# Performance work log

Measured on AMD Instinct MI355X. Metric: run time of the kernel, lower is better.

## Reference

```python
import jax, jax.numpy as jnp
import numpy as np

D_MODEL = 768
NUM_HEADS = 12
D_K = D_MODEL // NUM_HEADS


def setup_inputs() -> dict:
    key = jax.random.key(0)
    ks = jax.random.split(key, 12)
    B, S = 2, 2048
    s = 1.0 / np.sqrt(D_MODEL)
    inp = {
        "query": jax.random.normal(ks[0], (B, S, D_MODEL), jnp.float32),
        "key": jax.random.normal(ks[1], (B, S, D_MODEL), jnp.float32),
        "value": jax.random.normal(ks[2], (B, S, D_MODEL), jnp.float32),
        "mask": jnp.ones((B, 1, 1, S), jnp.int32),
        "Wq": jax.random.normal(ks[3], (D_MODEL, D_MODEL), jnp.float32) * s,
        "bq": jax.random.normal(ks[4], (D_MODEL,), jnp.float32) * s,
        "Wk": jax.random.normal(ks[5], (D_MODEL, D_MODEL), jnp.float32) * s,
        "bk": jax.random.normal(ks[6], (D_MODEL,), jnp.float32) * s,
        "Wv": jax.random.normal(ks[7], (D_MODEL, D_MODEL), jnp.float32) * s,
        "bv": jax.random.normal(ks[8], (D_MODEL,), jnp.float32) * s,
        "Wo": jax.random.normal(ks[9], (D_MODEL, D_MODEL), jnp.float32) * s,
        "bo": jax.random.normal(ks[10], (D_MODEL,), jnp.float32) * s,
    }
    return inp


def reference(query, key, value, mask, Wq, bq, Wk, bk, Wv, bv, Wo, bo):
    B, S, _ = query.shape
    def split_heads(x):  # [B,S,D] -> [B,H,S,d_k]
        return x.reshape(B, -1, NUM_HEADS, D_K).transpose(0, 2, 1, 3)
    q = split_heads(query @ Wq + bq)
    k = split_heads(key @ Wk + bk)
    v = split_heads(value @ Wv + bv)
    scores = jnp.einsum("bhqd,bhkd->bhqk", q, k) / jnp.sqrt(jnp.float32(D_K))
    scores = jnp.where(mask == 0, jnp.float32(-1e9), scores)
    attn = jax.nn.softmax(scores, axis=-1)
    # dropout omitted (eval/deterministic reference)
    out = jnp.einsum("bhqk,bhkd->bhqd", attn, v)
    out = out.transpose(0, 2, 1, 3).reshape(B, S, D_MODEL)
    return out @ Wo + bo
```

## Files before the change

kernel.cpp:

```cpp
#include <hip/hip_runtime.h>

#define DMODEL 768
#define NHEAD  12
#define DK     64
#define NB     2
#define SEQ    2048
#define NTOK   (NB*SEQ)
#define GKIT   (DMODEL/32)

using bf16x8 = __attribute__((ext_vector_type(8))) short;
using f32x4  = __attribute__((ext_vector_type(4))) float;

typedef __attribute__((address_space(1))) const unsigned int gas_u32;
typedef __attribute__((address_space(3))) unsigned int las_u32;

__device__ __forceinline__ void gload_lds16(const void* g, void* l) {
  __builtin_amdgcn_global_load_lds((gas_u32*)g, (las_u32*)l, 16, 0, 0);
}

__device__ __forceinline__ unsigned short f2bf(float f) {
  unsigned int u = __builtin_bit_cast(unsigned int, f);
  u = (u + 0x7FFFu + ((u >> 16) & 1u)) >> 16;
  return (unsigned short)u;
}

__device__ __forceinline__ unsigned cvtpk_bf16(float lo, float hi) {
  unsigned r;
  asm volatile("v_cvt_pk_bf16_f32 %0, %1, %2" : "=v"(r) : "v"(lo), "v"(hi));
  return r;
}

__device__ __forceinline__ unsigned exp2pk_bf16(float a, float b) {
  unsigned r;
  float t;
  asm volatile(
      "v_exp_f32 %0, %2\n\t"
      "v_exp_f32 %1, %3\n\t"
      "s_nop 0\n\t"
      "v_cvt_pk_bf16_f32 %0, %0, %1"
      : "=&v"(r), "=&v"(t)
      : "v"(a), "v"(b));
  return r;
}

__global__ __launch_bounds__(256) void prep_kernel(
    const float* __restrict__ q, const float* __restrict__ k, const float* __restrict__ v,
    unsigned short* __restrict__ oq, unsigned short* __restrict__ ok, unsigned short* __restrict__ ov,
    const float* __restrict__ w0, const float* __restrict__ w1,
    const float* __restrict__ w2, const float* __restrict__ w3,
    unsigned short* __restrict__ t0, unsigned short* __restrict__ t1,
    unsigned short* __restrict__ t2, unsigned short* __restrict__ t3,
    const int* __restrict__ mask, float* __restrict__ maskbias) {
  __shared__ unsigned short tile[64][80];
  int bid = blockIdx.x;
  int t = threadIdx.x;
  if (bid < 4608) {
    int z = bid / 1536, blk = bid % 1536;
    const float* in = z == 0 ? q : (z == 1 ? k : v);
    unsigned short* out = z == 0 ? oq : (z == 1 ? ok : ov);
    size_t i = ((size_t)blk * 256 + t) * 8;
    float4 f0 = *(const float4*)(in + i);
    float4 f1 = *(const float4*)(in + i + 4);
    uint4 w;
    w.x = cvtpk_bf16(f0.x, f0.y); w.y = cvtpk_bf16(f0.z, f0.w);
    w.z = cvtpk_bf16(f1.x, f1.y); w.w = cvtpk_bf16(f1.z, f1.w);
    *(uint4*)(out + i) = w;
  } else if (bid < 5328) {
    int wv = bid - 4608;
    int z = wv / 144, r = wv % 144;
    int c0 = (r % 12) * 64, r0 = (r / 12) * 64;
    const float* in = z == 0 ? w0 : z == 1 ? w1 : z == 2 ? w2 : w3;
    unsigned short* out = z == 0 ? t0 : z == 1 ? t1 : z == 2 ? t2 : t3;
    int row = t >> 2, ch = t & 3;
#pragma unroll
    for (int j4 = 0; j4 < 4; ++j4) {
      float4 f = *(const float4*)(in + (size_t)(r0 + row) * DMODEL + c0 + ch * 16 + j4 * 4);
      tile[row][ch * 16 + j4 * 4 + 0] = f2bf(f.x);
      tile[row][ch * 16 + j4 * 4 + 1] = f2bf(f.y);
      tile[row][ch * 16 + j4 * 4 + 2] = f2bf(f.z);
      tile[row][ch * 16 + j4 * 4 + 3] = f2bf(f.w);
    }
    __syncthreads();
    uint4 wA, wB;
    unsigned short* ta = (unsigned short*)&wA;
    unsigned short* tb = (unsigned short*)&wB;
#pragma unroll
    for (int j = 0; j < 8; ++j) { ta[j] = tile[ch * 16 + j][row]; tb[j] = tile[ch * 16 + 8 + j][row]; }
    unsigned short* ob = out + (size_t)(c0 + row) * DMODEL + r0 + ch * 16;
    *(uint4*)ob = wA;
    *(uint4*)(ob + 8) = wB;
  } else {
    for (int i = t; i < NB * SEQ; i += 256)
      maskbias[i] = mask[i] ? 0.f : -1.4426950408889634e9f;
  }
}

__device__ __forceinline__ void gemm_stage64(const unsigned short* A, const unsigned short* BT,
    unsigned short* As, unsigned short* Bs, int rowbase, int colbase, int kt, int wave, int lane) {
  int r = lane >> 2, c = lane & 3;
#pragma unroll
  for (int iss = 0; iss < 2; ++iss) {
    int row = wave * 32 + iss * 16 + r;
    gload_lds16(A + (size_t)(rowbase + row) * DMODEL + kt * 32 + c * 8,
                As + (wave * 32 + iss * 16) * 32);
  }
  int brow = wave * 16 + r;
  gload_lds16(BT + (size_t)(colbase + brow) * DMODEL + kt * 32 + c * 8, Bs + wave * 16 * 32);
}

__device__ __forceinline__ void gemm_core64(const unsigned short* A, const unsigned short* BT,
    char* gsm, int rowbase, int colbase, f32x4 acc[4][2]) {
  unsigned short* AsAll = (unsigned short*)gsm;
  unsigned short* BsAll = (unsigned short*)(gsm + 16384);
  int t = threadIdx.x, lane = t & 63, wave = t >> 6;
  int wr = wave >> 1, wc = wave & 1, l16 = lane & 15, lk = lane >> 4;
  gemm_stage64(A, BT, AsAll, BsAll, rowbase, colbase, 0, wave, lane);
  __builtin_amdgcn_sched_barrier(0);
  asm volatile("s_waitcnt vmcnt(0)" ::: "memory");
  __builtin_amdgcn_s_barrier();
  for (int kt = 0; kt < GKIT; ++kt) {
    int cur = kt & 1;
    if (kt < GKIT - 1) {
      gemm_stage64(A, BT, AsAll + (cur ^ 1) * 4096, BsAll + (cur ^ 1) * 2048,
                   rowbase, colbase, kt + 1, wave, lane);
      __builtin_amdgcn_sched_barrier(0);
      asm volatile("s_waitcnt vmcnt(3)" ::: "memory");
    } else {
      asm volatile("s_waitcnt vmcnt(0)" ::: "memory");
    }
    __builtin_amdgcn_s_barrier();
    __builtin_amdgcn_sched_barrier(0);
    unsigned short* As = AsAll + cur * 4096;
    unsigned short* Bs = BsAll + cur * 2048;
    bf16x8 a[4], bb[2];
#pragma unroll
    for (int m = 0; m < 4; ++m) a[m] = *(const bf16x8*)(As + (wr * 64 + m * 16 + l16) * 32 + lk * 8);
#pragma unroll
    for (int n = 0; n < 2; ++n) bb[n] = *(const bf16x8*)(Bs + (wc * 32 + n * 16 + l16) * 32 + lk * 8);
    __builtin_amdgcn_s_setprio(1);
#pragma unroll
    for (int m = 0; m < 4; ++m)
#pragma unroll
      for (int n = 0; n < 2; ++n)
        acc[m][n] = __builtin_amdgcn_mfma_f32_16x16x32_bf16(a[m], bb[n], acc[m][n], 0, 0, 0);
    __builtin_amdgcn_s_setprio(0);
    __builtin_amdgcn_sched_barrier(0);
    __builtin_amdgcn_s_barrier();
  }
}

struct QKVArgs {
  const unsigned short* A[3];
  const unsigned short* BT[3];
  const float* bias[3];
  unsigned short* out[3];
  float scale;
};

__global__ __launch_bounds__(256) void gemm_qkv_kernel(QKVArgs ga) {
  __shared__ char gsm[24576];
  int bid = blockIdx.x;
  int xcd = bid & 7, idx = bid >> 3;
  int rt = xcd * 4 + idx / 36;
  int ct = idx % 36;
  int z = ct / 12;
  int colbase = (ct % 12) * 64;
  int rowbase = rt * 128;
  f32x4 acc[4][2];
#pragma unroll
  for (int m = 0; m < 4; ++m)
#pragma unroll
    for (int n = 0; n < 2; ++n) acc[m][n] = (f32x4){0.f, 0.f, 0.f, 0.f};
  gemm_core64(ga.A[z], ga.BT[z], gsm, rowbase, colbase, acc);
  const float* bias = ga.bias[z];
  int t = threadIdx.x, lane = t & 63, wave = t >> 6;
  int wr = wave >> 1, wc = wave & 1, l16 = lane & 15, lk = lane >> 4;
  if (z == 2) {
    int hh = colbase >> 6;
#pragma unroll
    for (int n = 0; n < 2; ++n) {
      int c = wc * 32 + n * 16 + l16;
      float bv = bias[colbase + c];
      int swz = (c & 7) << 4;
#pragma unroll
      for (int m = 0; m < 4; ++m) {
        uint2 w;
        w.x = cvtpk_bf16(acc[m][n][0] + bv, acc[m][n][1] + bv);
        w.y = cvtpk_bf16(acc[m][n][2] + bv, acc[m][n][3] + bv);
        int rp = wr * 64 + m * 16 + lk * 4;
        *(uint2*)(gsm + c * 256 + ((rp * 2) ^ swz)) = w;
      }
    }
    __syncthreads();
    int c = t >> 2, ch = t & 3;
    int swz2 = (c & 7) << 4;
    int bb2 = rowbase >> 11;
    unsigned short* dst = ga.out[2] + ((size_t)(bb2 * NHEAD + hh) * DK + c) * SEQ +
                          (rowbase & 2047) + ch * 32;
#pragma unroll
    for (int j = 0; j < 4; ++j) {
      uint4 w = *(const uint4*)(gsm + c * 256 + ((ch * 64 + j * 16) ^ swz2));
      *(uint4*)(dst + j * 8) = w;
    }
  } else {
    float scale = (z == 0) ? ga.scale : 1.f;
    unsigned short* out = ga.out[z];
#pragma unroll
    for (int n = 0; n < 2; ++n) {
      int gcol = colbase + wc * 32 + n * 16 + l16;
      float bv = bias[gcol];
      int h = gcol >> 6, d = gcol & 63;
#pragma unroll
      for (int m = 0; m < 4; ++m) {
        int growb = rowbase + wr * 64 + m * 16 + lk * 4;
#pragma unroll
        for (int i = 0; i < 4; ++i) {
          int grow = growb + i;
          int b = grow >> 11, s = grow & 2047;
          out[((size_t)(b * NHEAD + h) * SEQ + s) * DK + d] = f2bf((acc[m][n][i] + bv) * scale);
        }
      }
    }
  }
}

__global__ __launch_bounds__(256) void gemm_o_kernel(
    const unsigned short* __restrict__ A, const unsigned short* __restrict__ BT,
    const float* __restrict__ bias, float* __restrict__ out) {
  __shared__ char gsm[24576];
  int bid = blockIdx.x;
  int xcd = bid & 7, idx = bid >> 3;
  int rt = xcd * 4 + idx / 12;
  int colbase = (idx % 12) * 64;
  int rowbase = rt * 128;
  f32x4 acc[4][2];
#pragma unroll
  for (int m = 0; m < 4; ++m)
#pragma unroll
    for (int n = 0; n < 2; ++n) acc[m][n] = (f32x4){0.f, 0.f, 0.f, 0.f};
  gemm_core64(A, BT, gsm, rowbase, colbase, acc);
  int lane = threadIdx.x & 63, wave = threadIdx.x >> 6;
  int wr = wave >> 1, wc = wave & 1, l16 = lane & 15, lk = lane >> 4;
#pragma unroll
  for (int n = 0; n < 2; ++n) {
    int gcol = colbase + wc * 32 + n * 16 + l16;
    float bv = bias[gcol];
#pragma unroll
    for (int m = 0; m < 4; ++m) {
      int growb = rowbase + wr * 64 + m * 16 + lk * 4;
#pragma unroll
      for (int i = 0; i < 4; ++i)
        out[(size_t)(growb + i) * DMODEL + gcol] = acc[m][n][i] + bv;
    }
  }
}

template<int SPLIT>
__global__ __launch_bounds__(256, 3) void flash_kernel(
    const unsigned short* __restrict__ Qh, const unsigned short* __restrict__ Kh,
    const unsigned short* __restrict__ Vt, const float* __restrict__ maskbias,
    unsigned short* __restrict__ AO, float* __restrict__ Opart, float* __restrict__ Lpart) {
  constexpr int NT = (SEQ / SPLIT) / 64;
  constexpr int MBI = (SPLIT == 2) ? 1 : 2;
  __shared__ char smem[49152 + MBI * 4096];
  char* Ks = smem;
  char* Vs = smem + 16384;
  char* Ps = smem + 32768;
  float* mbs = (float*)(smem + 49152);

  int orig = blockIdx.x;
  int xcd = orig & 7, idx = orig >> 3;
  int bh, qt, sp;
  if (SPLIT == 2) {
    bh = xcd * 3 + idx / 32;
    int r = idx & 31; qt = r >> 1; sp = r & 1;
  } else {
    bh = xcd * 3 + idx / 16;
    qt = idx & 15; sp = 0;
  }
  int b = bh / NHEAD, h = bh % NHEAD;
  int kv0 = sp * (SEQ / SPLIT);

  int t = threadIdx.x, lane = t & 63, wave = t >> 6;
  int l16 = lane & 15, lk = lane >> 4;
  size_t headQ = (size_t)bh * SEQ * DK;
  size_t headV = (size_t)bh * DK * SEQ;
  int qbase = qt * 128 + wave * 32;

  const unsigned short* Kg = Kh + headQ + (size_t)kv0 * DK;
  const unsigned short* Vg = Vt + headV + kv0;
  const float* mbg = maskbias + b * SEQ + kv0;
  char* Pw = Ps + wave * 4096;

  bf16x8 aq[2][2];
#pragma unroll
  for (int h2 = 0; h2 < 2; ++h2) {
    const unsigned short* qp = Qh + headQ + (size_t)(qbase + h2 * 16 + l16) * DK + lk * 8;
    aq[h2][0] = *(const bf16x8*)qp;
    aq[h2][1] = *(const bf16x8*)(qp + 32);
  }
  bf16x8 ones;
#pragma unroll
  for (int j = 0; j < 8; ++j) ones[j] = (short)0x3F80;

  int sr8 = lane >> 3, sch = lane & 7;
  const unsigned short* KgT = Kg + (size_t)(wave * 16 + sr8) * DK + ((sch ^ sr8) << 3);
  const unsigned short* VgT = Vg + (size_t)(wave * 16 + sr8) * SEQ + ((sch ^ sr8) << 3);
  char* kD0 = Ks + wave * 2048;
  char* vD0 = Vs + wave * 2048;

#pragma unroll
  for (int j = 0; j < MBI; ++j)
    gload_lds16(mbg + (wave * MBI + j) * 256 + lane * 4, (char*)mbs + (wave * MBI + j) * 1024);
  gload_lds16(KgT, kD0);
  gload_lds16(KgT + 512, kD0 + 1024);
  gload_lds16(VgT, vD0);
  gload_lds16(VgT + 8 * SEQ, vD0 + 1024);
  __builtin_amdgcn_sched_barrier(0);
  asm volatile("s_waitcnt vmcnt(0)" ::: "memory");
  __builtin_amdgcn_s_barrier();

  f32x4 o[2][4], lacc[2];
#pragma unroll
  for (int h2 = 0; h2 < 2; ++h2) {
    lacc[h2] = (f32x4){0.f, 0.f, 0.f, 0.f};
#pragma unroll
    for (int t4 = 0; t4 < 4; ++t4) o[h2][t4] = (f32x4){0.f, 0.f, 0.f, 0.f};
  }

  for (int kt = 0; kt < NT; ++kt) {
    int cur = kt & 1;
    if (kt + 1 < NT) {
      const unsigned short* kS = KgT + (size_t)(kt + 1) * 4096;
      const unsigned short* vS = VgT + (kt + 1) * 64;
      char* kD = kD0 + (cur ^ 1) * 8192;
      char* vD = vD0 + (cur ^ 1) * 8192;
      gload_lds16(kS, kD);
      gload_lds16(kS + 512, kD + 1024);
      gload_lds16(vS, vD);
      gload_lds16(vS + 8 * SEQ, vD + 1024);
      __builtin_amdgcn_sched_barrier(0);
      asm volatile("s_waitcnt vmcnt(4)" ::: "memory");
    } else {
      asm volatile("s_waitcnt vmcnt(0)" ::: "memory");
    }
    __builtin_amdgcn_s_barrier();
    __builtin_amdgcn_sched_barrier(0);

    const char* kb = Ks + cur * 8192;
    const char* vb = Vs + cur * 8192;

    f32x4 sv[2][4];
    __builtin_amdgcn_s_setprio(1);
#pragma unroll
    for (int n = 0; n < 4; ++n) {
      f32x4 bias = *(const f32x4*)((const char*)mbs + kt * 256 + n * 64 + lk * 16);
      int key = n * 16 + l16;
      bf16x8 k0 = *(const bf16x8*)(kb + ((key * 128 + lk * 16) ^ ((key & 7) << 4)));
      bf16x8 k1 = *(const bf16x8*)(kb + ((key * 128 + 64 + lk * 16) ^ ((key & 7) << 4)));
#pragma unroll
      for (int h2 = 0; h2 < 2; ++h2) {
        f32x4 zz = __builtin_amdgcn_mfma_f32_16x16x32_bf16(k1, aq[h2][1], bias, 0, 0, 0);
        sv[h2][n] = __builtin_amdgcn_mfma_f32_16x16x32_bf16(k0, aq[h2][0], zz, 0, 0, 0);
      }
    }
    __builtin_amdgcn_s_setprio(0);

#pragma unroll
    for (int h2 = 0; h2 < 2; ++h2)
#pragma unroll
      for (int n = 0; n < 4; ++n) {
        uint2 w;
        w.x = exp2pk_bf16(sv[h2][n][0], sv[h2][n][1]);
        w.y = exp2pk_bf16(sv[h2][n][2], sv[h2][n][3]);
        int qr = h2 * 16 + l16;
        int byt = (qr * 128 + n * 32 + lk * 8) ^ ((qr & 7) << 4);
        *(uint2*)(Pw + byt) = w;
      }

    bf16x8 ap[2][2];
#pragma unroll
    for (int h2 = 0; h2 < 2; ++h2) {
      int qr = h2 * 16 + l16;
      ap[h2][0] = *(const bf16x8*)(Pw + ((qr * 128 + lk * 16) ^ ((qr & 7) << 4)));
      ap[h2][1] = *(const bf16x8*)(Pw + ((qr * 128 + 64 + lk * 16) ^ ((qr & 7) << 4)));
    }

    __builtin_amdgcn_s_setprio(1);
#pragma unroll
    for (int t4 = 0; t4 < 4; ++t4) {
      int d = t4 * 16 + l16;
      bf16x8 bv0 = *(const bf16x8*)(vb + ((d * 128 + lk * 16) ^ ((d & 7) << 4)));
      bf16x8 bv1 = *(const bf16x8*)(vb + ((d * 128 + 64 + lk * 16) ^ ((d & 7) << 4)));
#pragma unroll
      for (int h2 = 0; h2 < 2; ++h2) {
        o[h2][t4] = __builtin_amdgcn_mfma_f32_16x16x32_bf16(ap[h2][0], bv0, o[h2][t4], 0, 0, 0);
        o[h2][t4] = __builtin_amdgcn_mfma_f32_16x16x32_bf16(ap[h2][1], bv1, o[h2][t4], 0, 0, 0);
      }
    }
#pragma unroll
    for (int h2 = 0; h2 < 2; ++h2) {
      lacc[h2] = __builtin_amdgcn_mfma_f32_16x16x32_bf16(ap[h2][0], ones, lacc[h2], 0, 0, 0);
      lacc[h2] = __builtin_amdgcn_mfma_f32_16x16x32_bf16(ap[h2][1], ones, lacc[h2], 0, 0, 0);
    }
    __builtin_amdgcn_s_setprio(0);
    __builtin_amdgcn_sched_barrier(0);
    __builtin_amdgcn_s_barrier();
  }

  if (SPLIT == 2) {
    size_t pb = ((size_t)(bh * 16 + qt) * 2 + sp) * 8192;
#pragma unroll
    for (int h2 = 0; h2 < 2; ++h2)
#pragma unroll
      for (int t4 = 0; t4 < 4; ++t4)
#pragma unroll
        for (int i = 0; i < 4; ++i)
          Opart[pb + (size_t)(wave * 32 + h2 * 16 + lk * 4 + i) * 64 + t4 * 16 + l16] = o[h2][t4][i];
    if (l16 == 0) {
      int qi0 = ((bh * 16 + qt) * 2 + sp) * 128 + wave * 32;
#pragma unroll
      for (int h2 = 0; h2 < 2; ++h2)
#pragma unroll
        for (int i = 0; i < 4; ++i)
          Lpart[qi0 + h2 * 16 + lk * 4 + i] = lacc[h2][i];
    }
  } else {
#pragma unroll
    for (int h2 = 0; h2 < 2; ++h2) {
      f32x4 li;
#pragma unroll
      for (int i = 0; i < 4; ++i) li[i] = 1.0f / lacc[h2][i];
#pragma unroll
      for (int t4 = 0; t4 < 4; ++t4) {
        int col = h * DK + t4 * 16 + l16;
#pragma unroll
        for (int i = 0; i < 4; ++i) {
          int srq = qbase + h2 * 16 + lk * 4 + i;
          AO[(size_t)(b * SEQ + srq) * DMODEL + col] = f2bf(o[h2][t4][i] * li[i]);
        }
      }
    }
  }
}

__global__ __launch_bounds__(256) void merge_kernel(
    const float* __restrict__ Opart, const float* __restrict__ Lpart,
    unsigned short* __restrict__ AO) {
  int blk = blockIdx.x;
  int qh = blk & 1;
  int qt = (blk >> 1) & 15;
  int bh = blk >> 5;
  int b = bh / NHEAD, h = bh % NHEAD;
  int t = threadIdx.x;
  int q = t >> 2, dc = (t & 3) * 16;
  size_t base0 = ((size_t)(bh * 16 + qt) * 2) * 8192 + (size_t)(qh * 64 + q) * 64 + dc;
  const float* o0 = Opart + base0;
  const float* o1 = o0 + 8192;
  int qi = (bh * 16 + qt) * 2 * 128 + qh * 64 + q;
  float l0 = Lpart[qi], l1 = Lpart[qi + 128];
  float linv = 1.f / (l0 + l1);
  int row = qt * 128 + qh * 64 + q;
  unsigned short* dst = AO + ((size_t)(b * SEQ + row)) * DMODEL + h * DK + dc;
#pragma unroll
  for (int j = 0; j < 4; ++j) {
    float4 a = *(const float4*)(o0 + j * 4);
    float4 c = *(const float4*)(o1 + j * 4);
    uint2 w;
    w.x = cvtpk_bf16((a.x + c.x) * linv, (a.y + c.y) * linv);
    w.y = cvtpk_bf16((a.z + c.z) * linv, (a.w + c.w) * linv);
    *(uint2*)(dst + j * 4) = w;
  }
}

extern "C" void kernel_launch(void* const* d_in, const int* in_sizes, int n_in,
                              void* d_out, int out_size, void* d_ws, size_t ws_size,
                              hipStream_t stream) {
  const float* gq  = (const float*)d_in[0];
  const float* gk  = (const float*)d_in[1];
  const float* gv  = (const float*)d_in[2];
  const int* gmask = (const int*)d_in[3];
  const float* gWq = (const float*)d_in[4];
  const float* gbq = (const float*)d_in[5];
  const float* gWk = (const float*)d_in[6];
  const float* gbk = (const float*)d_in[7];
  const float* gWv = (const float*)d_in[8];
  const float* gbv = (const float*)d_in[9];
  const float* gWo = (const float*)d_in[10];
  const float* gbo = (const float*)d_in[11];
  float* out = (float*)d_out;

  char* ws = (char*)d_ws;
  const size_t XSZ = (size_t)NTOK * DMODEL * 2;
  const size_t WSZ = (size_t)DMODEL * DMODEL * 2;
  const size_t OPSZ = (size_t)768 * 8192 * 4;

  float* Opart = (float*)ws;
  unsigned short* Xq = (unsigned short*)ws;
  unsigned short* Xk = Xq + XSZ / 2;
  unsigned short* Xv = Xk + XSZ / 2;
  char* p = ws + OPSZ;
  float* Lpart = (float*)p; p += (size_t)768 * 128 * 4;
  unsigned short* WqT = (unsigned short*)p; p += WSZ;
  unsigned short* WkT = (unsigned short*)p; p += WSZ;
  unsigned short* WvT = (unsigned short*)p; p += WSZ;
  unsigned short* WoT = (unsigned short*)p; p += WSZ;
  unsigned short* Qh  = (unsigned short*)p; p += XSZ;
  unsigned short* Kh  = (unsigned short*)p; p += XSZ;
  unsigned short* Vt  = (unsigned short*)p; p += XSZ;
  unsigned short* AO  = (unsigned short*)p; p += XSZ;
  float* maskbias     = (float*)p; p += (size_t)NB * SEQ * 4;
  size_t needed = (size_t)(p - ws);
  bool split2 = ws_size >= needed;

  prep_kernel<<<dim3(5329), 256, 0, stream>>>(gq, gk, gv, Xq, Xk, Xv,
                                              gWq, gWk, gWv, gWo, WqT, WkT, WvT, WoT,
                                              gmask, maskbias);

  QKVArgs ga;
  ga.A[0] = Xq; ga.A[1] = Xk; ga.A[2] = Xv;
  ga.BT[0] = WqT; ga.BT[1] = WkT; ga.BT[2] = WvT;
  ga.bias[0] = gbq; ga.bias[1] = gbk; ga.bias[2] = gbv;
  ga.out[0] = Qh; ga.out[1] = Kh; ga.out[2] = Vt;
  ga.scale = 0.18033688011112042f;
  gemm_qkv_kernel<<<dim3(1152), 256, 0, stream>>>(ga);

  if (split2) {
    flash_kernel<2><<<dim3(768), 256, 0, stream>>>(Qh, Kh, Vt, maskbias, AO, Opart, Lpart);
    merge_kernel<<<dim3(768), 256, 0, stream>>>(Opart, Lpart, AO);
  } else {
    flash_kernel<1><<<dim3(384), 256, 0, stream>>>(Qh, Kh, Vt, maskbias, AO, Opart, Lpart);
  }
  gemm_o_kernel<<<dim3(384), 256, 0, stream>>>(AO, WoT, gbo, out);
}
```

Baseline: 108.6 us.

## Double GEMM K-tile to 64 with XOR-swizzled LDS layout

The QKV and output projection GEMMs now stage 64-wide K slices per iteration instead of 32. This halves the number of main-loop iterations and barriers. The LDS tile uses an XOR swizzle on 16-byte chunks to avoid bank conflicts on the MFMA operand reads. Shared memory doubles to 48KB, and an occupancy hint of 3 blocks is added, which may limit residency. An extra sync was added before the V epilogue reuses the shared buffer.

```diff
diff --git a/kernel.cpp b/kernel.cpp
--- a/kernel.cpp
+++ b/kernel.cpp
@@ -6,7 +6,7 @@
 #define NB     2
 #define SEQ    2048
 #define NTOK   (NB*SEQ)
-#define GKIT   (DMODEL/32)
+#define GK64   (DMODEL/64)
 
 using bf16x8 = __attribute__((ext_vector_type(8))) short;
 using f32x4  = __attribute__((ext_vector_type(4))) float;
@@ -97,52 +97,68 @@
 
 __device__ __forceinline__ void gemm_stage64(const unsigned short* A, const unsigned short* BT,
     unsigned short* As, unsigned short* Bs, int rowbase, int colbase, int kt, int wave, int lane) {
-  int r = lane >> 2, c = lane & 3;
-#pragma unroll
-  for (int iss = 0; iss < 2; ++iss) {
-    int row = wave * 32 + iss * 16 + r;
-    gload_lds16(A + (size_t)(rowbase + row) * DMODEL + kt * 32 + c * 8,
-                As + (wave * 32 + iss * 16) * 32);
-  }
-  int brow = wave * 16 + r;
-  gload_lds16(BT + (size_t)(colbase + brow) * DMODEL + kt * 32 + c * 8, Bs + wave * 16 * 32);
+  int r8 = lane >> 3, c = lane & 7;
+  int swz = (c ^ r8) << 3;
+#pragma unroll
+  for (int g = 0; g < 4; ++g) {
+    int row = wave * 32 + g * 8 + r8;
+    gload_lds16(A + (size_t)(rowbase + row) * DMODEL + kt * 64 + swz,
+                As + (wave * 32 + g * 8) * 64);
+  }
+#pragma unroll
+  for (int g = 0; g < 2; ++g) {
+    int row = wave * 16 + g * 8 + r8;
+    gload_lds16(BT + (size_t)(colbase + row) * DMODEL + kt * 64 + swz,
+                Bs + (wave * 16 + g * 8) * 64);
+  }
 }
 
 __device__ __forceinline__ void gemm_core64(const unsigned short* A, const unsigned short* BT,
     char* gsm, int rowbase, int colbase, f32x4 acc[4][2]) {
   unsigned short* AsAll = (unsigned short*)gsm;
-  unsigned short* BsAll = (unsigned short*)(gsm + 16384);
+  unsigned short* BsAll = (unsigned short*)(gsm + 32768);
   int t = threadIdx.x, lane = t & 63, wave = t >> 6;
   int wr = wave >> 1, wc = wave & 1, l16 = lane & 15, lk = lane >> 4;
   gemm_stage64(A, BT, AsAll, BsAll, rowbase, colbase, 0, wave, lane);
   __builtin_amdgcn_sched_barrier(0);
   asm volatile("s_waitcnt vmcnt(0)" ::: "memory");
   __builtin_amdgcn_s_barrier();
-  for (int kt = 0; kt < GKIT; ++kt) {
+  for (int kt = 0; kt < GK64; ++kt) {
     int cur = kt & 1;
-    if (kt < GKIT - 1) {
-      gemm_stage64(A, BT, AsAll + (cur ^ 1) * 4096, BsAll + (cur ^ 1) * 2048,
+    if (kt < GK64 - 1) {
+      gemm_stage64(A, BT, AsAll + (cur ^ 1) * 8192, BsAll + (cur ^ 1) * 4096,
                    rowbase, colbase, kt + 1, wave, lane);
       __builtin_amdgcn_sched_barrier(0);
-      asm volatile("s_waitcnt vmcnt(3)" ::: "memory");
+      asm volatile("s_waitcnt vmcnt(6)" ::: "memory");
     } else {
       asm volatile("s_waitcnt vmcnt(0)" ::: "memory");
     }
     __builtin_amdgcn_s_barrier();
     __builtin_amdgcn_sched_barrier(0);
-    unsigned short* As = AsAll + cur * 4096;
-    unsigned short* Bs = BsAll + cur * 2048;
-    bf16x8 a[4], bb[2];
-#pragma unroll
-    for (int m = 0; m < 4; ++m) a[m] = *(const bf16x8*)(As + (wr * 64 + m * 16 + l16) * 32 + lk * 8);
-#pragma unroll
-    for (int n = 0; n < 2; ++n) bb[n] = *(const bf16x8*)(Bs + (wc * 32 + n * 16 + l16) * 32 + lk * 8);
+    const char* As = (const char*)(AsAll + cur * 8192);
+    const char* Bs = (const char*)(BsAll + cur * 4096);
+    bf16x8 a[2][4], bb[2][2];
+#pragma unroll
+    for (int k2 = 0; k2 < 2; ++k2) {
+#pragma unroll
+      for (int m = 0; m < 4; ++m) {
+        int row = wr * 64 + m * 16 + l16;
+        a[k2][m] = *(const bf16x8*)(As + row * 128 + (((k2 * 4 + lk) ^ (row & 7)) << 4));
+      }
+#pragma unroll
+      for (int n = 0; n < 2; ++n) {
+        int row = wc * 32 + n * 16 + l16;
+        bb[k2][n] = *(const bf16x8*)(Bs + row * 128 + (((k2 * 4 + lk) ^ (row & 7)) << 4));
+      }
+    }
     __builtin_amdgcn_s_setprio(1);
 #pragma unroll
-    for (int m = 0; m < 4; ++m)
-#pragma unroll
-      for (int n = 0; n < 2; ++n)
-        acc[m][n] = __builtin_amdgcn_mfma_f32_16x16x32_bf16(a[m], bb[n], acc[m][n], 0, 0, 0);
+    for (int k2 = 0; k2 < 2; ++k2)
+#pragma unroll
+      for (int m = 0; m < 4; ++m)
+#pragma unroll
+        for (int n = 0; n < 2; ++n)
+          acc[m][n] = __builtin_amdgcn_mfma_f32_16x16x32_bf16(a[k2][m], bb[k2][n], acc[m][n], 0, 0, 0);
     __builtin_amdgcn_s_setprio(0);
     __builtin_amdgcn_sched_barrier(0);
     __builtin_amdgcn_s_barrier();
@@ -157,8 +173,8 @@
   float scale;
 };
 
-__global__ __launch_bounds__(256) void gemm_qkv_kernel(QKVArgs ga) {
-  __shared__ char gsm[24576];
+__global__ __launch_bounds__(256, 3) void gemm_qkv_kernel(QKVArgs ga) {
+  __shared__ char gsm[49152];
   int bid = blockIdx.x;
   int xcd = bid & 7, idx = bid >> 3;
   int rt = xcd * 4 + idx / 36;
@@ -176,6 +192,7 @@
   int t = threadIdx.x, lane = t & 63, wave = t >> 6;
   int wr = wave >> 1, wc = wave & 1, l16 = lane & 15, lk = lane >> 4;
   if (z == 2) {
+    __syncthreads();
     int hh = colbase >> 6;
 #pragma unroll
     for (int n = 0; n < 2; ++n) {
@@ -224,10 +241,10 @@
   }
 }
 
-__global__ __launch_bounds__(256) void gemm_o_kernel(
+__global__ __launch_bounds__(256, 3) void gemm_o_kernel(
     const unsigned short* __restrict__ A, const unsigned short* __restrict__ BT,
     const float* __restrict__ bias, float* __restrict__ out) {
-  __shared__ char gsm[24576];
+  __shared__ char gsm[49152];
   int bid = blockIdx.x;
   int xcd = bid & 7, idx = bid >> 3;
   int rt = xcd * 4 + idx / 12;
```

New measurement: 96.72 us. -10.9%, faster.
